# Kernel tuning notes

Measured on AMD Instinct MI355X. Metric: run time of the kernel, lower is better.

## Reference

```python
import jax, jax.numpy as jnp
import numpy as np

L = 3          # num_layers
H = 128        # hidden_dim
NH = 4         # num heads
DH = H // NH   # head dim
B = 32         # graphs per batch
N = 1024       # nodes per graph
NTOT = B * N
DEG = 16
E = NTOT * DEG
BN_EPS = 1e-5


def setup_inputs() -> dict:
    key = jax.random.key(0)
    ks = jax.random.split(key, 16)
    s = 1.0 / np.sqrt(H)
    inp = {
        "x": jax.random.normal(ks[0], (NTOT, H), jnp.float32),
        "edge_attr": jax.random.normal(ks[1], (E, H), jnp.float32),
        "gine_w1": jax.random.normal(ks[2], (L, H, H), jnp.float32) * s,
        "gine_b1": jnp.zeros((L, H), jnp.float32),
        "gine_bn_g": jnp.ones((L, H), jnp.float32),
        "gine_bn_b": jnp.zeros((L, H), jnp.float32),
        "gine_w2": jax.random.normal(ks[3], (L, H, H), jnp.float32) * s,
        "gine_b2": jnp.zeros((L, H), jnp.float32),
        "attn_wqkv": jax.random.normal(ks[4], (L, 3 * H, H), jnp.float32) * s,
        "attn_bqkv": jnp.zeros((L, 3 * H), jnp.float32),
        "attn_wo": jax.random.normal(ks[5], (L, H, H), jnp.float32) * s,
        "attn_bo": jnp.zeros((L, H), jnp.float32),
        "norm1_g": jnp.ones((L, H), jnp.float32),
        "norm1_b": jnp.zeros((L, H), jnp.float32),
        "norm2_g": jnp.ones((L, H), jnp.float32),
        "norm2_b": jnp.zeros((L, H), jnp.float32),
        "norm3_g": jnp.ones((L, H), jnp.float32),
        "norm3_b": jnp.zeros((L, H), jnp.float32),
        "mlp_w1": jax.random.normal(ks[6], (L, 2 * H, H), jnp.float32) * s,
        "mlp_b1": jnp.zeros((L, 2 * H), jnp.float32),
        "mlp_w2": jax.random.normal(ks[7], (L, H, 2 * H), jnp.float32) * (1.0 / np.sqrt(2 * H)),
        "mlp_b2": jnp.zeros((L, H), jnp.float32),
    }
    # intra-graph random edges: local src/dst in [0, N) plus per-graph offset
    offs = (jnp.arange(E, dtype=jnp.int32) // (N * DEG)) * N  # graph offset per edge
    src = jax.random.randint(ks[8], (E,), 0, N, jnp.int32) + offs
    dst = jax.random.randint(ks[9], (E,), 0, N, jnp.int32) + offs
    inp["edge_index"] = jnp.stack([src, dst]).astype(jnp.int32)
    inp["batch"] = (jnp.arange(NTOT, dtype=jnp.int32) // N)
    return inp


def _bn(x, g, b):
    m = x.mean(axis=0)
    v = jnp.var(x, axis=0)
    return (x - m) * jax.lax.rsqrt(v + BN_EPS) * g + b


def _gps_forward(x, edge_attr, gine_w1, gine_b1, gine_bn_g, gine_bn_b, gine_w2, gine_b2,
                 attn_wqkv, attn_bqkv, attn_wo, attn_bo,
                 norm1_g, norm1_b, norm2_g, norm2_b, norm3_g, norm3_b,
                 mlp_w1, mlp_b1, mlp_w2, mlp_b2, edge_index, batch):
    src, dst = edge_index[0], edge_index[1]
    for i in range(L):
        # ---- GINEConv: msg = relu(x_j + e), sum-scatter, nn-MLP on x + aggr (eps=0)
        msg = jax.nn.relu(x[src] + edge_attr)                       # [E, H]
        aggr = jax.ops.segment_sum(msg, dst, num_segments=NTOT)     # [NTOT, H]
        h = x + aggr
        h = h @ gine_w1[i].T + gine_b1[i]
        h = jax.nn.relu(_bn(h, gine_bn_g[i], gine_bn_b[i]))
        h = h @ gine_w2[i].T + gine_b2[i]
        h_local = _bn(h + x, norm1_g[i], norm1_b[i])                # residual + norm1
        # ---- global multi-head attention on x (dense per-graph, equal sizes)
        xb = x.reshape(B, N, H)
        qkv = xb @ attn_wqkv[i].T + attn_bqkv[i]                    # [B, N, 3H]
        q, k, v = jnp.split(qkv, 3, axis=-1)
        q = q.reshape(B, N, NH, DH).transpose(0, 2, 1, 3)           # [B, nh, N, dh]
        k = k.reshape(B, N, NH, DH).transpose(0, 2, 1, 3)
        v = v.reshape(B, N, NH, DH).transpose(0, 2, 1, 3)
        scores = jnp.einsum("bhqd,bhkd->bhqk", q, k) / np.sqrt(DH)
        attn = jax.nn.softmax(scores, axis=-1)
        o = jnp.einsum("bhqk,bhkd->bhqd", attn, v)
        o = o.transpose(0, 2, 1, 3).reshape(B, N, H) @ attn_wo[i].T + attn_bo[i]
        h_attn = _bn(o.reshape(NTOT, H) + x, norm2_g[i], norm2_b[i])
        # ---- combine + FFN + norm3
        out = h_local + h_attn
        ff = jax.nn.relu(out @ mlp_w1[i].T + mlp_b1[i]) @ mlp_w2[i].T + mlp_b2[i]
        x = _bn(out + ff, norm3_g[i], norm3_b[i])
        if i != L - 1:
            x = jax.nn.relu(x)
    return x


def reference(x, edge_attr, gine_w1, gine_b1, gine_bn_g, gine_bn_b, gine_w2, gine_b2,
              attn_wqkv, attn_bqkv, attn_wo, attn_bo,
              norm1_g, norm1_b, norm2_g, norm2_b, norm3_g, norm3_b,
              mlp_w1, mlp_b1, mlp_w2, mlp_b2, edge_index, batch):
    return _gps_forward(x, edge_attr, gine_w1, gine_b1, gine_bn_g, gine_bn_b, gine_w2, gine_b2,
                        attn_wqkv, attn_bqkv, attn_wo, attn_bo,
                        norm1_g, norm1_b, norm2_g, norm2_b, norm3_g, norm3_b,
                        mlp_w1, mlp_b1, mlp_w2, mlp_b2, edge_index, batch)
```

## Files before the change

### kernel.cpp

```cpp
#include <hip/hip_runtime.h>
#include <hip/hip_bf16.h>
#include <math.h>

#define NTOT 32768
#define HDIM 128
#define NE   524288
#define NGRAPH 32
#define NNODE 1024
#define NHEAD 4
#define DHEAD 32

typedef __attribute__((ext_vector_type(8))) short bf8v;
typedef __attribute__((ext_vector_type(4))) float f4v;
typedef unsigned short u16;

__device__ __forceinline__ float4 ld4(const float* p){ return *(const float4*)p; }

__device__ __forceinline__ u16 bf16rn(float f){
  union { float f; unsigned u; } x; x.f = f;
  unsigned r = x.u + 0x7FFF + ((x.u >> 16) & 1);
  return (u16)(r >> 16);
}
__device__ __forceinline__ unsigned pk2(float a, float b){
  unsigned r;
  asm("v_cvt_pk_bf16_f32 %0, %1, %2" : "=v"(r) : "v"(a), "v"(b));
  return r;
}
__device__ __forceinline__ float bf2f(u16 u){
  union { unsigned u; float f; } x; x.u = ((unsigned)u) << 16;
  return x.f;
}

__global__ void k_count(const int* __restrict__ dst, int* __restrict__ deg){
  int e = blockIdx.x*256 + threadIdx.x;
  atomicAdd(&deg[dst[e]], 1);
}

__global__ __launch_bounds__(1024) void k_scan(const int* __restrict__ deg,
                                               int* __restrict__ indptr,
                                               int* __restrict__ cursor){
  __shared__ int sm[1024];
  int t = threadIdx.x;
  int base = t*32;
  int s = 0;
  for (int j=0;j<32;j++) s += deg[base+j];
  sm[t] = s; __syncthreads();
  for (int off=1; off<1024; off<<=1){
    int v = (t>=off) ? sm[t-off] : 0;
    __syncthreads();
    sm[t] += v;
    __syncthreads();
  }
  int ex = sm[t] - s;
  for (int j=0;j<32;j++){
    int d = deg[base+j];
    indptr[base+j] = ex; cursor[base+j] = ex;
    ex += d;
  }
  if (t == 1023) indptr[NTOT] = ex;
}

__global__ void k_fill(const int* __restrict__ dst, int* __restrict__ cursor,
                       int* __restrict__ epos){
  int e = blockIdx.x*256 + threadIdx.x;
  int pos = atomicAdd(&cursor[dst[e]], 1);
  epos[e] = pos;
}

__global__ __launch_bounds__(256) void k_prep(const float* __restrict__ ea,
    const int* __restrict__ src, const int* __restrict__ epos,
    u16* __restrict__ EAb, int* __restrict__ SRCp,
    const float* __restrict__ x, u16* __restrict__ Xb,
    const float* s0,const float* s1,const float* s2,
    const float* s3,const float* s4,const float* s5, u16* __restrict__ Wb){
  int b = blockIdx.x, tid = threadIdx.x;
  if (b < 65536){
    int e = b*8 + (tid>>5);
    int c4 = (tid&31)*4;
    int pos = epos[e];
    float4 v = ld4(&ea[(size_t)e*HDIM + c4]);
    uint2 o; o.x = pk2(v.x, v.y); o.y = pk2(v.z, v.w);
    *(uint2*)&EAb[(size_t)pos*HDIM + c4] = o;
    if ((tid&31) == 0) SRCp[pos] = src[e];
  } else if (b < 69632){
    size_t i = ((size_t)(b-65536)*256 + tid)*4;
    float4 v = ld4(&x[i]);
    uint2 o; o.x = pk2(v.x,v.y); o.y = pk2(v.z,v.w);
    *(uint2*)&Xb[i] = o;
  } else {
    int idx = b - 69632;
    int y = idx / 144;
    int i = (idx % 144)*256 + tid;
    const float* srcs[6] = {s0,s1,s2,s3,s4,s5};
    const int cnt4[6] = {12288,12288,36864,12288,24576,24576};
    const int off[6]  = {0,49152,98304,245760,294912,393216};
    if (i < cnt4[y]){
      float4 v = ld4(&srcs[y][(size_t)i*4]);
      uint2 o; o.x = pk2(v.x,v.y); o.y = pk2(v.z,v.w);
      *(uint2*)&Wb[off[y] + (size_t)i*4] = o;
    }
  }
}

__device__ __forceinline__ void aggr_body(int bx, int tid,
    const u16* __restrict__ Xb, const u16* __restrict__ EAb,
    const int* __restrict__ SRCp, const int* __restrict__ indptr,
    u16* __restrict__ Hb){
  int n = bx*8 + (tid>>5);
  int c4 = (tid&31)*4;
  int p0 = indptr[n], p1 = indptr[n+1];
  float a0=0.f,a1=0.f,a2=0.f,a3=0.f;
  int p = p0;
  int sNext = (p < p1) ? SRCp[p] : 0;
  for (; p<p1; p++){
    int s = sNext;
    if (p+1 < p1) sNext = SRCp[p+1];
    uint2 ev = *(const uint2*)&EAb[(size_t)p*HDIM + c4];
    uint2 xv = *(const uint2*)&Xb[(size_t)s*HDIM + c4];
    a0 += fmaxf(bf2f((u16)(xv.x&0xffff)) + bf2f((u16)(ev.x&0xffff)), 0.f);
    a1 += fmaxf(bf2f((u16)(xv.x>>16))    + bf2f((u16)(ev.x>>16)), 0.f);
    a2 += fmaxf(bf2f((u16)(xv.y&0xffff)) + bf2f((u16)(ev.y&0xffff)), 0.f);
    a3 += fmaxf(bf2f((u16)(xv.y>>16))    + bf2f((u16)(ev.y>>16)), 0.f);
  }
  uint2 xn = *(const uint2*)&Xb[(size_t)n*HDIM + c4];
  a0 += bf2f((u16)(xn.x&0xffff)); a1 += bf2f((u16)(xn.x>>16));
  a2 += bf2f((u16)(xn.y&0xffff)); a3 += bf2f((u16)(xn.y>>16));
  uint2 o; o.x = pk2(a0,a1); o.y = pk2(a2,a3);
  *(uint2*)&Hb[(size_t)n*HDIM + c4] = o;
}

template<bool BNA, bool DUAL, bool RELU, bool EP, bool STATS, bool WROUT>
__device__ __forceinline__ void bgemm_body(int bx, int by, int tid,
    const u16* __restrict__ Ab, const u16* __restrict__ A2b,
    const float* __restrict__ slotA, const float* __restrict__ gA, const float* __restrict__ bA,
    const float* __restrict__ slotB, const float* __restrict__ gB, const float* __restrict__ bB,
    const u16* __restrict__ Wb, const float* __restrict__ bias,
    const u16* __restrict__ Epb, u16* __restrict__ Cb,
    u16* __restrict__ OUTb, float* __restrict__ slotOut, int N, int K,
    float* sbn1, float* sbn2, float* sred){
  int w = tid>>6, l = tid&63;
  int q = l&15, g = l>>4;
  int m0 = bx*128, n0 = by*64;
  int wr = w*32;
  const float invn = 1.0f/32768.0f;
  if ((BNA || DUAL) && tid < 128){
    float mean = slotA[tid]*invn;
    float var  = slotA[128+tid]*invn - mean*mean;
    float s = gA[tid] * rsqrtf(var + 1e-5f);
    sbn1[tid] = s; sbn1[128+tid] = bA[tid] - mean*s;
    if (DUAL){
      float mean2 = slotB[tid]*invn;
      float var2  = slotB[128+tid]*invn - mean2*mean2;
      float s2 = gB[tid] * rsqrtf(var2 + 1e-5f);
      sbn2[tid] = s2; sbn2[128+tid] = bB[tid] - mean2*s2;
    }
  }
  if (STATS && tid < 128) sred[tid] = 0.f;
  if (BNA || DUAL || STATS) __syncthreads();

  f4v acc[2][4];
  #pragma unroll
  for (int i=0;i<2;i++)
    #pragma unroll
    for (int j=0;j<4;j++) acc[i][j] = (f4v){0.f,0.f,0.f,0.f};

  for (int kc=0; kc<K; kc+=32){
    bf8v af[2];
    #pragma unroll
    for (int mt=0;mt<2;mt++){
      int row = m0 + wr + 16*mt + q;
      if (!BNA && !DUAL){
        af[mt] = *(const bf8v*)&Ab[(size_t)row*K + kc + 8*g];
      } else {
        union { bf8v b; u16 s[8]; unsigned u[4]; } ra, r2, ro;
        ra.b = *(const bf8v*)&Ab[(size_t)row*K + kc + 8*g];
        if (DUAL) r2.b = *(const bf8v*)&A2b[(size_t)row*K + kc + 8*g];
        float v[8];
        #pragma unroll
        for (int j=0;j<8;j++){
          int kk = kc + 8*g + j;
          float f = bf2f(ra.s[j]) * sbn1[kk] + sbn1[128+kk];
          if (BNA) f = fmaxf(f, 0.f);
          if (DUAL) f += bf2f(r2.s[j]) * sbn2[kk] + sbn2[128+kk];
          v[j] = f;
        }
        ro.u[0]=pk2(v[0],v[1]); ro.u[1]=pk2(v[2],v[3]);
        ro.u[2]=pk2(v[4],v[5]); ro.u[3]=pk2(v[6],v[7]);
        af[mt] = ro.b;
        if (WROUT && by == 0)
          *(uint4*)&OUTb[(size_t)row*K + kc + 8*g] = *(uint4*)ro.u;
      }
    }
    bf8v bfv[4];
    #pragma unroll
    for (int nt=0;nt<4;nt++)
      bfv[nt] = *(const bf8v*)&Wb[(size_t)(n0+16*nt+q)*K + kc + 8*g];
    #pragma unroll
    for (int mt=0;mt<2;mt++)
      #pragma unroll
      for (int nt=0;nt<4;nt++)
        acc[mt][nt] = __builtin_amdgcn_mfma_f32_16x16x32_bf16(af[mt], bfv[nt], acc[mt][nt], 0,0,0);
  }
  float bbv[4];
  #pragma unroll
  for (int nt=0;nt<4;nt++) bbv[nt] = bias[n0 + 16*nt + q];
  float csum[4] = {0.f,0.f,0.f,0.f}, csq[4] = {0.f,0.f,0.f,0.f};
  #pragma unroll
  for (int mt=0;mt<2;mt++){
    int row0 = m0 + wr + 16*mt + 4*g;
    #pragma unroll
    for (int nt=0;nt<4;nt++){
      int col = n0 + 16*nt + q;
      #pragma unroll
      for (int r=0;r<4;r++){
        size_t off = (size_t)(row0+r)*N + col;
        float v = acc[mt][nt][r] + bbv[nt];
        if (EP) v += bf2f(Epb[off]);
        if (RELU) v = fmaxf(v, 0.f);
        Cb[off] = bf16rn(v);
        if (STATS){ csum[nt] += v; csq[nt] += v*v; }
      }
    }
  }
  if (STATS){
    #pragma unroll
    for (int nt=0;nt<4;nt++){
      int c = 16*nt + q;
      atomicAdd(&sred[c], csum[nt]);
      atomicAdd(&sred[64+c], csq[nt]);
    }
    __syncthreads();
    if (tid < 64){
      atomicAdd(&slotOut[n0+tid], sred[tid]);
      atomicAdd(&slotOut[128+n0+tid], sred[64+tid]);
    }
  }
}

__device__ __forceinline__ void qkv_body(int bx, int by, int tid,
    const u16* __restrict__ Ab, const u16* __restrict__ Wb, const float* __restrict__ bias,
    u16* __restrict__ Qb, u16* __restrict__ Kb, u16* __restrict__ VT, u16* Sm){
  int w = tid>>6, l = tid&63;
  int q = l&15, g = l>>4;
  int which = by >> 1, half = by & 1;
  int m0 = bx*128, n0 = by*64;
  const int K = 128;
  int wr = w*32;
  f4v acc[2][4];
  #pragma unroll
  for (int i=0;i<2;i++)
    #pragma unroll
    for (int j=0;j<4;j++) acc[i][j] = (f4v){0.f,0.f,0.f,0.f};
  for (int kc=0; kc<K; kc+=32){
    bf8v af[2];
    #pragma unroll
    for (int mt=0;mt<2;mt++)
      af[mt] = *(const bf8v*)&Ab[(size_t)(m0+wr+16*mt+q)*K + kc + 8*g];
    bf8v bfv[4];
    #pragma unroll
    for (int nt=0;nt<4;nt++)
      bfv[nt] = *(const bf8v*)&Wb[(size_t)(n0+16*nt+q)*K + kc + 8*g];
    #pragma unroll
    for (int mt=0;mt<2;mt++)
      #pragma unroll
      for (int nt=0;nt<4;nt++)
        acc[mt][nt] = __builtin_amdgcn_mfma_f32_16x16x32_bf16(af[mt], bfv[nt], acc[mt][nt], 0,0,0);
  }
  const float QSC = 0.17677669529663687f * 1.4426950408889634f;
  float scale = (which==0) ? QSC : 1.0f;
  float bbv[4];
  #pragma unroll
  for (int nt=0;nt<4;nt++) bbv[nt] = bias[n0 + 16*nt + q];
  if (which < 2){
    #pragma unroll
    for (int mt=0;mt<2;mt++){
      int row0 = wr + 16*mt + 4*g;
      #pragma unroll
      for (int nt=0;nt<4;nt++){
        int c = 16*nt + q;
        #pragma unroll
        for (int r=0;r<4;r++)
          Sm[(row0+r)*72 + c] = bf16rn((acc[mt][nt][r] + bbv[nt]) * scale);
      }
    }
    __syncthreads();
    u16* dst = (which==0) ? Qb : Kb;
    #pragma unroll
    for (int it=0; it<4; it++){
      int idx = tid + it*256;
      int row = idx >> 3, c8 = (idx & 7) * 8;
      uint4 v = *(const uint4*)&Sm[row*72 + c8];
      *(uint4*)&dst[(size_t)(m0+row)*128 + half*64 + c8] = v;
    }
  } else {
    #pragma unroll
    for (int mt=0;mt<2;mt++){
      int row0 = wr + 16*mt + 4*g;
      #pragma unroll
      for (int nt=0;nt<4;nt++){
        int c = 16*nt + q;
        uint2 p;
        p.x = pk2(acc[mt][nt][0] + bbv[nt], acc[mt][nt][1] + bbv[nt]);
        p.y = pk2(acc[mt][nt][2] + bbv[nt], acc[mt][nt][3] + bbv[nt]);
        *(uint2*)&Sm[c*136 + row0] = p;
      }
    }
    __syncthreads();
    int gg = m0 >> 10;
    int nl0 = m0 & 1023;
    #pragma unroll
    for (int it=0; it<4; it++){
      int idx = tid + it*256;
      int c = idx >> 4, n8 = (idx & 15) * 8;
      uint4 v = *(const uint4*)&Sm[c*136 + n8];
      *(uint4*)&VT[((size_t)gg*128 + half*64 + c)*1024 + nl0 + n8] = v;
    }
  }
}

__device__ __forceinline__ void flash_body(int qt, int h, int g, int tid,
    const u16* __restrict__ Qb, const u16* __restrict__ Kb, const u16* __restrict__ VT,
    u16* __restrict__ O, u16* Pl){
  int w = tid >> 6, l = tid & 63;
  int q = l & 15, grp = l >> 4;
  size_t gbase = (size_t)g*1024;
  size_t qrow0 = gbase + qt*64 + w*16;
  const u16* Vp = VT + ((size_t)(g*4 + h)*32)*1024;
  bf8v qf = *(const bf8v*)&Qb[(qrow0 + q)*128 + h*32 + 8*grp];
  u16* Pw = Pl + w*(16*72);
  float m = -1e30f, lsum = 0.f;
  f4v o0 = {0.f,0.f,0.f,0.f}, o1 = {0.f,0.f,0.f,0.f};
  for (int kt=0; kt<16; kt++){
    int k0 = kt*64;
    f4v st[4];
    #pragma unroll
    for (int t=0;t<4;t++){
      bf8v kf = *(const bf8v*)&Kb[(gbase + k0 + 16*t + q)*128 + h*32 + 8*grp];
      st[t] = __builtin_amdgcn_mfma_f32_16x16x32_bf16(kf, qf, (f4v){0.f,0.f,0.f,0.f}, 0,0,0);
    }
    float smax = st[0][0];
    #pragma unroll
    for (int t=0;t<4;t++)
      #pragma unroll
      for (int r=0;r<4;r++) smax = fmaxf(smax, st[t][r]);
    smax = fmaxf(smax, __shfl_xor(smax, 16));
    smax = fmaxf(smax, __shfl_xor(smax, 32));
    bool need = __any(smax > m + 8.f);
    float mnew = m, alpha = 1.f;
    if (need){
      mnew = fmaxf(m, smax);
      alpha = exp2f(m - mnew);
    }
    float psum = 0.f;
    #pragma unroll
    for (int t=0;t<4;t++){
      float p0 = exp2f(st[t][0]-mnew), p1 = exp2f(st[t][1]-mnew);
      float p2 = exp2f(st[t][2]-mnew), p3 = exp2f(st[t][3]-mnew);
      psum += (p0+p1)+(p2+p3);
      *(unsigned*)&Pw[q*72 + 16*t + 4*grp]     = pk2(p0,p1);
      *(unsigned*)&Pw[q*72 + 16*t + 4*grp + 2] = pk2(p2,p3);
    }
    psum += __shfl_xor(psum, 16);
    psum += __shfl_xor(psum, 32);
    lsum = lsum*alpha + psum;
    m = mnew;
    if (need){
      f4v aD;
      #pragma unroll
      for (int r=0;r<4;r++) aD[r] = __shfl(alpha, 4*grp + r);
      #pragma unroll
      for (int r=0;r<4;r++){ o0[r] *= aD[r]; o1[r] *= aD[r]; }
    }
    bf8v pa0 = *(const bf8v*)&Pw[q*72 + 8*grp];
    bf8v pa1 = *(const bf8v*)&Pw[q*72 + 32 + 8*grp];
    bf8v v00 = *(const bf8v*)&Vp[(size_t)q*1024      + k0 + 8*grp];
    bf8v v01 = *(const bf8v*)&Vp[(size_t)q*1024      + k0 + 32 + 8*grp];
    bf8v v10 = *(const bf8v*)&Vp[(size_t)(16+q)*1024 + k0 + 8*grp];
    bf8v v11 = *(const bf8v*)&Vp[(size_t)(16+q)*1024 + k0 + 32 + 8*grp];
    o0 = __builtin_amdgcn_mfma_f32_16x16x32_bf16(pa0, v00, o0, 0,0,0);
    o0 = __builtin_amdgcn_mfma_f32_16x16x32_bf16(pa1, v01, o0, 0,0,0);
    o1 = __builtin_amdgcn_mfma_f32_16x16x32_bf16(pa0, v10, o1, 0,0,0);
    o1 = __builtin_amdgcn_mfma_f32_16x16x32_bf16(pa1, v11, o1, 0,0,0);
  }
  f4v lD;
  #pragma unroll
  for (int r=0;r<4;r++) lD[r] = __shfl(lsum, 4*grp + r);
  #pragma unroll
  for (int r=0;r<4;r++){
    float inv = 1.0f/lD[r];
    size_t row = qrow0 + 4*grp + r;
    O[row*HDIM + h*32 + q]      = bf16rn(o0[r]*inv);
    O[row*HDIM + h*32 + 16 + q] = bf16rn(o1[r]*inv);
  }
}

__global__ __launch_bounds__(256) void k_d1(const u16* __restrict__ Xb,
    const u16* __restrict__ EAb, const int* __restrict__ SRCp, const int* __restrict__ indptr,
    u16* __restrict__ Hb,
    const u16* __restrict__ wq, const float* __restrict__ BQ,
    u16* __restrict__ Qb, u16* __restrict__ Kb, u16* __restrict__ VTb){
  __shared__ u16 Sm[128*72];
  int bx = blockIdx.x;
  if (bx < 4096){
    aggr_body(bx, threadIdx.x, Xb, EAb, SRCp, indptr, Hb);
  } else {
    int b = bx - 4096;
    qkv_body(b & 255, b >> 8, threadIdx.x, Xb, wq, BQ, Qb, Kb, VTb, Sm);
  }
}

__global__ __launch_bounds__(256) void k_d2(const u16* __restrict__ Qb,
    const u16* __restrict__ Kb, const u16* __restrict__ VTb, u16* __restrict__ Ob,
    const u16* __restrict__ Hb, const u16* __restrict__ w1, const float* __restrict__ B1,
    u16* __restrict__ G1, float* __restrict__ S0){
  __shared__ u16 Pl[4*16*72];
  __shared__ float sb1[256], sb2[256], sr[128];
  int bx = blockIdx.x;
  if (bx < 2048){
    flash_body(bx & 15, (bx >> 4) & 3, bx >> 6, threadIdx.x, Qb, Kb, VTb, Ob, Pl);
  } else {
    int b = bx - 2048;
    bgemm_body<false,false,false,false,true,false>(b & 255, b >> 8, threadIdx.x,
      Hb, nullptr, nullptr,nullptr,nullptr, nullptr,nullptr,nullptr,
      w1, B1, nullptr, G1, nullptr, S0, 128, 128, sb1, sb2, sr);
  }
}

__global__ __launch_bounds__(256) void k_d3(const u16* __restrict__ G1,
    const float* __restrict__ S0, const float* __restrict__ bnG, const float* __restrict__ bnB,
    const u16* __restrict__ w2, const float* __restrict__ B2,
    const u16* __restrict__ Xb, u16* __restrict__ P1, float* __restrict__ S1,
    const u16* __restrict__ Ob, const u16* __restrict__ wo, const float* __restrict__ BO,
    u16* __restrict__ P2, float* __restrict__ S2){
  __shared__ float sb1[256], sb2[256], sr[128];
  int bx = blockIdx.x;
  if (bx < 512){
    bgemm_body<true,false,false,true,true,false>(bx & 255, bx >> 8, threadIdx.x,
      G1, nullptr, S0, bnG, bnB, nullptr,nullptr,nullptr,
      w2, B2, Xb, P1, nullptr, S1, 128, 128, sb1, sb2, sr);
  } else {
    int b = bx - 512;
    bgemm_body<false,false,false,true,true,false>(b & 255, b >> 8, threadIdx.x,
      Ob, nullptr, nullptr,nullptr,nullptr, nullptr,nullptr,nullptr,
      wo, BO, Xb, P2, nullptr, S2, 128, 128, sb1, sb2, sr);
  }
}

__global__ __launch_bounds__(256) void k_mlpf(const u16* __restrict__ P1, const u16* __restrict__ P2,
    const float* __restrict__ S1, const float* __restrict__ n1g, const float* __restrict__ n1b,
    const float* __restrict__ S2, const float* __restrict__ n2g, const float* __restrict__ n2b,
    const u16* __restrict__ wm1, const float* __restrict__ BM1,
    const u16* __restrict__ wm2, const float* __restrict__ BM2,
    u16* __restrict__ H3, float* __restrict__ S3){
  __shared__ u16 FF[64][268];
  __shared__ u16 OUTs[64][138];
  __shared__ float sb1[256], sb2[256], sred[256];
  int tid = threadIdx.x;
  int w = tid>>6, l = tid&63;
  int q = l&15, g = l>>4;
  int m0 = blockIdx.x*64;
  const float invn = 1.0f/32768.0f;
  if (tid < 128){
    float mean = S1[tid]*invn;
    float var  = S1[128+tid]*invn - mean*mean;
    float s = n1g[tid] * rsqrtf(var + 1e-5f);
    sb1[tid] = s; sb1[128+tid] = n1b[tid] - mean*s;
    float mean2 = S2[tid]*invn;
    float var2  = S2[128+tid]*invn - mean2*mean2;
    float s2 = n2g[tid] * rsqrtf(var2 + 1e-5f);
    sb2[tid] = s2; sb2[128+tid] = n2b[tid] - mean2*s2;
    sred[tid] = 0.f; sred[128+tid] = 0.f;
  }
  __syncthreads();

  f4v acc1[16];
  #pragma unroll
  for (int j=0;j<16;j++) acc1[j] = (f4v){0.f,0.f,0.f,0.f};
  int lrow = w*16 + q;
  int row = m0 + lrow;
  for (int kc=0; kc<128; kc+=32){
    union { bf8v b; u16 s[8]; unsigned u[4]; } ra, r2, ro;
    ra.b = *(const bf8v*)&P1[(size_t)row*128 + kc + 8*g];
    r2.b = *(const bf8v*)&P2[(size_t)row*128 + kc + 8*g];
    float v[8];
    #pragma unroll
    for (int j=0;j<8;j++){
      int kk = kc + 8*g + j;
      v[j] = bf2f(ra.s[j]) * sb1[kk] + sb1[128+kk]
           + bf2f(r2.s[j]) * sb2[kk] + sb2[128+kk];
    }
    ro.u[0]=pk2(v[0],v[1]); ro.u[1]=pk2(v[2],v[3]);
    ro.u[2]=pk2(v[4],v[5]); ro.u[3]=pk2(v[6],v[7]);
    *(uint4*)&OUTs[lrow][kc + 8*g] = *(uint4*)ro.u;
    #pragma unroll
    for (int nt=0;nt<16;nt++){
      bf8v bv = *(const bf8v*)&wm1[(size_t)(16*nt+q)*128 + kc + 8*g];
      acc1[nt] = __builtin_amdgcn_mfma_f32_16x16x32_bf16(ro.b, bv, acc1[nt], 0,0,0);
    }
  }
  #pragma unroll
  for (int nt=0;nt<16;nt++){
    int col = 16*nt + q;
    float bb = BM1[col];
    int r0 = w*16 + 4*g;
    #pragma unroll
    for (int r=0;r<4;r++)
      FF[r0+r][col] = bf16rn(fmaxf(acc1[nt][r] + bb, 0.f));
  }
  __syncthreads();

  f4v acc2[8];
  #pragma unroll
  for (int j=0;j<8;j++) acc2[j] = (f4v){0.f,0.f,0.f,0.f};
  for (int kc=0; kc<256; kc+=32){
    bf8v af = *(const bf8v*)&FF[lrow][kc + 8*g];
    #pragma unroll
    for (int nt=0;nt<8;nt++){
      bf8v bv = *(const bf8v*)&wm2[(size_t)(16*nt+q)*256 + kc + 8*g];
      acc2[nt] = __builtin_amdgcn_mfma_f32_16x16x32_bf16(af, bv, acc2[nt], 0,0,0);
    }
  }
  float csum[8], csq[8];
  #pragma unroll
  for (int nt=0;nt<8;nt++){ csum[nt]=0.f; csq[nt]=0.f; }
  int r0 = w*16 + 4*g;
  #pragma unroll
  for (int nt=0;nt<8;nt++){
    int col = 16*nt + q;
    float bb = BM2[col];
    #pragma unroll
    for (int r=0;r<4;r++){
      float v = acc2[nt][r] + bb + bf2f(OUTs[r0+r][col]);
      H3[(size_t)(m0+r0+r)*128 + col] = bf16rn(v);
      csum[nt] += v; csq[nt] += v*v;
    }
  }
  #pragma unroll
  for (int nt=0;nt<8;nt++){
    int c = 16*nt + q;
    atomicAdd(&sred[c], csum[nt]);
    atomicAdd(&sred[128+c], csq[nt]);
  }
  __syncthreads();
  if (tid < 128){
    atomicAdd(&S3[tid], sred[tid]);
    atomicAdd(&S3[128+tid], sred[128+tid]);
  }
}

template<bool RELU, bool F32OUT>
__global__ __launch_bounds__(256) void k_bnapply(const u16* __restrict__ X,
    const float* __restrict__ slot, const float* __restrict__ gv, const float* __restrict__ bv,
    u16* __restrict__ Yb, float* __restrict__ Yf){
  int idx = blockIdx.x*256 + threadIdx.x;
  int row = idx >> 4, c8 = (idx & 15) * 8;
  const float invn = 1.0f/32768.0f;
  union { uint4 u; u16 s[8]; } iv;
  iv.u = *(const uint4*)&X[(size_t)row*HDIM + c8];
  float o[8];
  #pragma unroll
  for (int j=0;j<8;j++){
    int c = c8+j;
    float mean = slot[c]*invn;
    float var  = slot[128+c]*invn - mean*mean;
    float sc = gv[c] * rsqrtf(var + 1e-5f);
    float sh = bv[c] - mean*sc;
    float v = bf2f(iv.s[j])*sc + sh;
    if (RELU) v = fmaxf(v, 0.f);
    o[j] = v;
  }
  if (F32OUT){
    float* dst = &Yf[(size_t)row*HDIM + c8];
    *(float4*)dst = make_float4(o[0],o[1],o[2],o[3]);
    *(float4*)(dst+4) = make_float4(o[4],o[5],o[6],o[7]);
  } else {
    uint4 ov;
    ov.x = pk2(o[0],o[1]); ov.y = pk2(o[2],o[3]);
    ov.z = pk2(o[4],o[5]); ov.w = pk2(o[6],o[7]);
    *(uint4*)&Yb[(size_t)row*HDIM + c8] = ov;
  }
}

extern "C" void kernel_launch(void* const* d_in, const int* in_sizes, int n_in,
                              void* d_out, int out_size, void* d_ws, size_t ws_size,
                              hipStream_t stream){
  const float* x_in      = (const float*)d_in[0];
  const float* edge_attr = (const float*)d_in[1];
  const float* gine_w1   = (const float*)d_in[2];
  const float* gine_b1   = (const float*)d_in[3];
  const float* gine_bn_g = (const float*)d_in[4];
  const float* gine_bn_b = (const float*)d_in[5];
  const float* gine_w2   = (const float*)d_in[6];
  const float* gine_b2   = (const float*)d_in[7];
  const float* attn_wqkv = (const float*)d_in[8];
  const float* attn_bqkv = (const float*)d_in[9];
  const float* attn_wo   = (const float*)d_in[10];
  const float* attn_bo   = (const float*)d_in[11];
  const float* norm1_g   = (const float*)d_in[12];
  const float* norm1_b   = (const float*)d_in[13];
  const float* norm2_g   = (const float*)d_in[14];
  const float* norm2_b   = (const float*)d_in[15];
  const float* norm3_g   = (const float*)d_in[16];
  const float* norm3_b   = (const float*)d_in[17];
  const float* mlp_w1    = (const float*)d_in[18];
  const float* mlp_b1    = (const float*)d_in[19];
  const float* mlp_w2    = (const float*)d_in[20];
  const float* mlp_b2    = (const float*)d_in[21];
  const int* edge_index  = (const int*)d_in[22];
  const int* srcp = edge_index;
  const int* dstp = edge_index + NE;
  float* out = (float*)d_out;

  float* ws = (float*)d_ws;
  const size_t U = 4194304;
  u16* Xb   = (u16*)(ws);
  u16* Hb   = (u16*)(ws + U/2);
  u16* G1   = (u16*)(ws + U);
  u16* P1   = (u16*)(ws + U + U/2);
  u16* P2   = (u16*)(ws + 2*U);
  u16* Ob   = (u16*)(ws + 2*U + U/2);
  u16* H3   = (u16*)(ws + 3*U);
  u16* Qb   = (u16*)(ws + 5*U);
  u16* Kb   = (u16*)(ws + 5*U + U/2);
  u16* VTb  = (u16*)(ws + 6*U);
  u16* Wball= (u16*)(ws + 6*U + U/2);
  float* STATS = ws + 7*U - 8192;
  int* IW      = (int*)(ws + 7*U);
  int* deg     = IW;
  int* indptr  = IW + 32768;
  int* cursor  = IW + 32768 + 32772;
  int* epos    = cursor + 32768;
  u16* EAb  = (u16*)(ws + 8*U);
  int* SRCp = (int*)(ws + 16*U);

  u16* W1b  = Wball + 0;
  u16* W2b  = Wball + 49152;
  u16* WQb  = Wball + 98304;
  u16* WOb  = Wball + 245760;
  u16* WM1b = Wball + 294912;
  u16* WM2b = Wball + 393216;

  hipMemsetAsync(STATS, 0, 8192*sizeof(float) + NTOT*sizeof(int), stream);
  k_count<<<NE/256, 256, 0, stream>>>(dstp, deg);
  k_scan<<<1, 1024, 0, stream>>>(deg, indptr, cursor);
  k_fill<<<NE/256, 256, 0, stream>>>(dstp, cursor, epos);
  k_prep<<<70496, 256, 0, stream>>>(edge_attr, srcp, epos, EAb, SRCp, x_in, Xb,
                                    gine_w1, gine_w2, attn_wqkv, attn_wo, mlp_w1, mlp_w2, Wball);

  for (int i=0;i<3;i++){
    const float* B1 = gine_b1 + (size_t)i*HDIM;
    const float* B2 = gine_b2 + (size_t)i*HDIM;
    const float* BQ = attn_bqkv + (size_t)i*3*HDIM;
    const float* BO = attn_bo + (size_t)i*HDIM;
    const float* BM1 = mlp_b1 + (size_t)i*2*HDIM;
    const float* BM2 = mlp_b2 + (size_t)i*HDIM;
    u16* w1 = W1b + (size_t)i*16384;
    u16* w2 = W2b + (size_t)i*16384;
    u16* wq = WQb + (size_t)i*49152;
    u16* wo = WOb + (size_t)i*16384;
    u16* wm1 = WM1b + (size_t)i*32768;
    u16* wm2 = WM2b + (size_t)i*32768;
    float* S0 = STATS + (size_t)(i*4+0)*512;
    float* S1 = STATS + (size_t)(i*4+1)*512;
    float* S2 = STATS + (size_t)(i*4+2)*512;
    float* S3 = STATS + (size_t)(i*4+3)*512;
    const float* bnG = gine_bn_g + (size_t)i*HDIM;
    const float* bnB = gine_bn_b + (size_t)i*HDIM;
    const float* n1g = norm1_g + (size_t)i*HDIM, *n1b = norm1_b + (size_t)i*HDIM;
    const float* n2g = norm2_g + (size_t)i*HDIM, *n2b = norm2_b + (size_t)i*HDIM;
    const float* n3g = norm3_g + (size_t)i*HDIM, *n3b = norm3_b + (size_t)i*HDIM;

    k_d1<<<5632, 256, 0, stream>>>(Xb, EAb, SRCp, indptr, Hb, wq, BQ, Qb, Kb, VTb);
    k_d2<<<2560, 256, 0, stream>>>(Qb, Kb, VTb, Ob, Hb, w1, B1, G1, S0);
    k_d3<<<1024, 256, 0, stream>>>(G1, S0, bnG, bnB, w2, B2, Xb, P1, S1,
                                   Ob, wo, BO, P2, S2);
    k_mlpf<<<512, 256, 0, stream>>>(P1, P2, S1, n1g, n1b, S2, n2g, n2b,
                                    wm1, BM1, wm2, BM2, H3, S3);

    if (i<2) k_bnapply<true ,false><<<2048, 256, 0, stream>>>(H3, S3, n3g, n3b, Xb, nullptr);
    else     k_bnapply<false,true ><<<2048, 256, 0, stream>>>(H3, S3, n3g, n3b, nullptr, out);
  }
}
```

Before: 979.0 us.

## Split flash attention KV range across warps and software-prefetch K tiles

The flash-attention part of k_d2 now uses 32-row query tiles, with two warps per row group each covering half of the key range. The partial outputs, maxima and sums are merged through shared memory using a log-sum-exp rescale. K fragments for the next tile are prefetched into registers and V loads are issued earlier in each iteration to hide latency, and launch bounds request 4 blocks per CU. This doubles the flash block count for more parallelism, at the cost of extra shared memory, a block barrier and a merge step.

After: 977.0 us. No clear change (-0.2%).

```diff
diff --git a/kernel.cpp b/kernel.cpp
--- a/kernel.cpp
+++ b/kernel.cpp
@@ -320,29 +320,51 @@
 
 __device__ __forceinline__ void flash_body(int qt, int h, int g, int tid,
     const u16* __restrict__ Qb, const u16* __restrict__ Kb, const u16* __restrict__ VT,
-    u16* __restrict__ O, u16* Pl){
+    u16* __restrict__ O, u16* Pl, float* Om, float* Ml){
   int w = tid >> 6, l = tid & 63;
   int q = l & 15, grp = l >> 4;
+  int rh = w & 1, kh = w >> 1;
   size_t gbase = (size_t)g*1024;
-  size_t qrow0 = gbase + qt*64 + w*16;
+  size_t qrow0 = gbase + qt*32 + rh*16;
   const u16* Vp = VT + ((size_t)(g*4 + h)*32)*1024;
   bf8v qf = *(const bf8v*)&Qb[(qrow0 + q)*128 + h*32 + 8*grp];
   u16* Pw = Pl + w*(16*72);
+  float* Omw = Om + w*(16*32);
+  float* Mlw = Ml + w*32;
   float m = -1e30f, lsum = 0.f;
   f4v o0 = {0.f,0.f,0.f,0.f}, o1 = {0.f,0.f,0.f,0.f};
-  for (int kt=0; kt<16; kt++){
-    int k0 = kt*64;
+  int kt0 = kh*8;
+  bf8v kf0, kf1, kf2, kf3;
+  {
+    int k0 = kt0*64;
+    kf0 = *(const bf8v*)&Kb[(gbase + k0 +  0 + q)*128 + h*32 + 8*grp];
+    kf1 = *(const bf8v*)&Kb[(gbase + k0 + 16 + q)*128 + h*32 + 8*grp];
+    kf2 = *(const bf8v*)&Kb[(gbase + k0 + 32 + q)*128 + h*32 + 8*grp];
+    kf3 = *(const bf8v*)&Kb[(gbase + k0 + 48 + q)*128 + h*32 + 8*grp];
+  }
+  for (int it=0; it<8; it++){
+    int k0 = (kt0+it)*64;
+    bf8v v00 = *(const bf8v*)&Vp[(size_t)q*1024      + k0 + 8*grp];
+    bf8v v01 = *(const bf8v*)&Vp[(size_t)q*1024      + k0 + 32 + 8*grp];
+    bf8v v10 = *(const bf8v*)&Vp[(size_t)(16+q)*1024 + k0 + 8*grp];
+    bf8v v11 = *(const bf8v*)&Vp[(size_t)(16+q)*1024 + k0 + 32 + 8*grp];
     f4v st[4];
-    #pragma unroll
-    for (int t=0;t<4;t++){
-      bf8v kf = *(const bf8v*)&Kb[(gbase + k0 + 16*t + q)*128 + h*32 + 8*grp];
-      st[t] = __builtin_amdgcn_mfma_f32_16x16x32_bf16(kf, qf, (f4v){0.f,0.f,0.f,0.f}, 0,0,0);
-    }
-    float smax = st[0][0];
-    #pragma unroll
-    for (int t=0;t<4;t++)
-      #pragma unroll
-      for (int r=0;r<4;r++) smax = fmaxf(smax, st[t][r]);
+    st[0] = __builtin_amdgcn_mfma_f32_16x16x32_bf16(kf0, qf, (f4v){0.f,0.f,0.f,0.f}, 0,0,0);
+    st[1] = __builtin_amdgcn_mfma_f32_16x16x32_bf16(kf1, qf, (f4v){0.f,0.f,0.f,0.f}, 0,0,0);
+    st[2] = __builtin_amdgcn_mfma_f32_16x16x32_bf16(kf2, qf, (f4v){0.f,0.f,0.f,0.f}, 0,0,0);
+    st[3] = __builtin_amdgcn_mfma_f32_16x16x32_bf16(kf3, qf, (f4v){0.f,0.f,0.f,0.f}, 0,0,0);
+    if (it < 7){
+      int kn = k0 + 64;
+      kf0 = *(const bf8v*)&Kb[(gbase + kn +  0 + q)*128 + h*32 + 8*grp];
+      kf1 = *(const bf8v*)&Kb[(gbase + kn + 16 + q)*128 + h*32 + 8*grp];
+      kf2 = *(const bf8v*)&Kb[(gbase + kn + 32 + q)*128 + h*32 + 8*grp];
+      kf3 = *(const bf8v*)&Kb[(gbase + kn + 48 + q)*128 + h*32 + 8*grp];
+    }
+    float ma = fmaxf(fmaxf(st[0][0],st[0][1]), fmaxf(st[0][2],st[0][3]));
+    float mb = fmaxf(fmaxf(st[1][0],st[1][1]), fmaxf(st[1][2],st[1][3]));
+    float mc = fmaxf(fmaxf(st[2][0],st[2][1]), fmaxf(st[2][2],st[2][3]));
+    float md = fmaxf(fmaxf(st[3][0],st[3][1]), fmaxf(st[3][2],st[3][3]));
+    float smax = fmaxf(fmaxf(ma,mb), fmaxf(mc,md));
     smax = fmaxf(smax, __shfl_xor(smax, 16));
     smax = fmaxf(smax, __shfl_xor(smax, 32));
     bool need = __any(smax > m + 8.f);
@@ -373,24 +395,42 @@
     }
     bf8v pa0 = *(const bf8v*)&Pw[q*72 + 8*grp];
     bf8v pa1 = *(const bf8v*)&Pw[q*72 + 32 + 8*grp];
-    bf8v v00 = *(const bf8v*)&Vp[(size_t)q*1024      + k0 + 8*grp];
-    bf8v v01 = *(const bf8v*)&Vp[(size_t)q*1024      + k0 + 32 + 8*grp];
-    bf8v v10 = *(const bf8v*)&Vp[(size_t)(16+q)*1024 + k0 + 8*grp];
-    bf8v v11 = *(const bf8v*)&Vp[(size_t)(16+q)*1024 + k0 + 32 + 8*grp];
     o0 = __builtin_amdgcn_mfma_f32_16x16x32_bf16(pa0, v00, o0, 0,0,0);
     o0 = __builtin_amdgcn_mfma_f32_16x16x32_bf16(pa1, v01, o0, 0,0,0);
     o1 = __builtin_amdgcn_mfma_f32_16x16x32_bf16(pa0, v10, o1, 0,0,0);
     o1 = __builtin_amdgcn_mfma_f32_16x16x32_bf16(pa1, v11, o1, 0,0,0);
   }
-  f4v lD;
-  #pragma unroll
-  for (int r=0;r<4;r++) lD[r] = __shfl(lsum, 4*grp + r);
+  if (grp == 0){ Mlw[q] = lsum; Mlw[16+q] = m; }
   #pragma unroll
   for (int r=0;r<4;r++){
-    float inv = 1.0f/lD[r];
-    size_t row = qrow0 + 4*grp + r;
-    O[row*HDIM + h*32 + q]      = bf16rn(o0[r]*inv);
-    O[row*HDIM + h*32 + 16 + q] = bf16rn(o1[r]*inv);
+    Omw[(4*grp+r)*32 + q]      = o0[r];
+    Omw[(4*grp+r)*32 + 16 + q] = o1[r];
+  }
+  __syncthreads();
+  if (kh == 0){
+    const float* Mlo = Ml + (w+2)*32;
+    const float* Omo = Om + (w+2)*(16*32);
+    float m_ot = Mlo[16+q];
+    float l_ot = Mlo[q];
+    float mstar = fmaxf(m, m_ot);
+    float a_me = exp2f(m - mstar), a_ot = exp2f(m_ot - mstar);
+    float lstar = lsum*a_me + l_ot*a_ot;
+    f4v aMe, aOt, lD;
+    #pragma unroll
+    for (int r=0;r<4;r++){
+      aMe[r] = __shfl(a_me, 4*grp + r);
+      aOt[r] = __shfl(a_ot, 4*grp + r);
+      lD[r]  = __shfl(lstar, 4*grp + r);
+    }
+    #pragma unroll
+    for (int r=0;r<4;r++){
+      float v0 = o0[r]*aMe[r] + Omo[(4*grp+r)*32 + q]*aOt[r];
+      float v1 = o1[r]*aMe[r] + Omo[(4*grp+r)*32 + 16 + q]*aOt[r];
+      float inv = 1.0f/lD[r];
+      size_t row = qrow0 + 4*grp + r;
+      O[row*HDIM + h*32 + q]      = bf16rn(v0*inv);
+      O[row*HDIM + h*32 + 16 + q] = bf16rn(v1*inv);
+    }
   }
 }
 
@@ -409,17 +449,20 @@
   }
 }
 
-__global__ __launch_bounds__(256) void k_d2(const u16* __restrict__ Qb,
+__global__ __launch_bounds__(256,4) void k_d2(const u16* __restrict__ Qb,
     const u16* __restrict__ Kb, const u16* __restrict__ VTb, u16* __restrict__ Ob,
     const u16* __restrict__ Hb, const u16* __restrict__ w1, const float* __restrict__ B1,
     u16* __restrict__ G1, float* __restrict__ S0){
   __shared__ u16 Pl[4*16*72];
+  __shared__ float Om[4*16*32];
+  __shared__ float Ml[4*32];
   __shared__ float sb1[256], sb2[256], sr[128];
   int bx = blockIdx.x;
-  if (bx < 2048){
-    flash_body(bx & 15, (bx >> 4) & 3, bx >> 6, threadIdx.x, Qb, Kb, VTb, Ob, Pl);
+  if (bx < 4096){
+    int qt = bx & 31, h = (bx >> 5) & 3, g = bx >> 7;
+    flash_body(qt, h, g, threadIdx.x, Qb, Kb, VTb, Ob, Pl, Om, Ml);
   } else {
-    int b = bx - 2048;
+    int b = bx - 4096;
     bgemm_body<false,false,false,false,true,false>(b & 255, b >> 8, threadIdx.x,
       Hb, nullptr, nullptr,nullptr,nullptr, nullptr,nullptr,nullptr,
       w1, B1, nullptr, G1, nullptr, S0, 128, 128, sb1, sb2, sr);
@@ -671,7 +714,7 @@
     const float* n3g = norm3_g + (size_t)i*HDIM, *n3b = norm3_b + (size_t)i*HDIM;
 
     k_d1<<<5632, 256, 0, stream>>>(Xb, EAb, SRCp, indptr, Hb, wq, BQ, Qb, Kb, VTb);
-    k_d2<<<2560, 256, 0, stream>>>(Qb, Kb, VTb, Ob, Hb, w1, B1, G1, S0);
+    k_d2<<<4608, 256, 0, stream>>>(Qb, Kb, VTb, Ob, Hb, w1, B1, G1, S0);
     k_d3<<<1024, 256, 0, stream>>>(G1, S0, bnG, bnB, w2, B2, Xb, P1, S1,
                                    Ob, wo, BO, P2, S2);
     k_mlpf<<<512, 256, 0, stream>>>(P1, P2, S1, n1g, n1b, S2, n2g, n2b,
```
